# Performance work log

Hardware: AMD Instinct MI355X
Metric: run time of the kernel (lower is better)

## Reference

```python
import jax, jax.numpy as jnp
import numpy as np

B, T, U, E, P, C = 32, 4096, 1024, 512, 512, 4
LN_EPS = 1e-5


def setup_inputs() -> dict:
    key = jax.random.key(0)
    k = jax.random.split(key, 6)
    enc_out = jax.random.normal(k[0], (B, T, E), dtype=jnp.float32)
    pred_out = jax.random.normal(k[1], (B, U, P), dtype=jnp.float32)
    frame_label = jax.random.randint(k[2], (B, T), 0, C)
    frame_tlabel = jax.random.randint(k[3], (B, U), 0, C)
    # every emotion id appears in each sample's label list (dense [B, C])
    label = jnp.tile(jnp.arange(C), (B, 1))
    # LayerNorm params (torch defaults: weight=1, bias=0)
    norm_w = jnp.ones((E + P,), dtype=jnp.float32)
    norm_b = jnp.zeros((E + P,), dtype=jnp.float32)
    # Linear head params
    head_w = jax.random.normal(k[4], (C, E + P), dtype=jnp.float32) * 0.02
    head_b = jnp.zeros((C,), dtype=jnp.float32)
    return {
        "enc_out": enc_out, "pred_out": pred_out,
        "frame_label": frame_label, "frame_tlabel": frame_tlabel,
        "label": label,
        "norm_w": norm_w, "norm_b": norm_b,
        "head_w": head_w, "head_b": head_b,
    }


def _masked_mean(x, ids, n_cls):
    # x: [B, S, D]; ids: [B, S] -> per-class mean [B, C, D] via one-hot segment-sum
    onehot = (ids[:, :, None] == jnp.arange(n_cls)[None, None, :]).astype(x.dtype)  # [B,S,C]
    cnt = onehot.sum(axis=1)                                   # [B, C]
    summed = jnp.einsum('bsc,bsd->bcd', onehot, x)             # [B, C, D]
    return summed / jnp.maximum(cnt, 1.0)[..., None]


def reference(enc_out, pred_out, frame_label, frame_tlabel, label, norm_w, norm_b, head_w, head_b):
    n_cls = head_w.shape[0]
    enc_mean = _masked_mean(enc_out, frame_label, n_cls)    # [B, C, E]
    pred_mean = _masked_mean(pred_out, frame_tlabel, n_cls)  # [B, C, P]
    feat = jnp.concatenate([enc_mean, pred_mean], axis=-1)   # [B, C, E+P]
    # LayerNorm over last dim
    mu = feat.mean(axis=-1, keepdims=True)
    var = jnp.mean((feat - mu) ** 2, axis=-1, keepdims=True)
    feat_n = (feat - mu) / jnp.sqrt(var + LN_EPS) * norm_w + norm_b
    logits = jnp.einsum('bcd,nd->bcn', feat_n, head_w) + head_b  # [B, C, n_cls]
    logp = jax.nn.log_softmax(logits, axis=-1)
    # loss += -log_softmax(head(norm(cat)))[emo] for each emo in label[i]
    bb, ll = label.shape
    sel = logp[jnp.arange(bb)[:, None], label, label]  # [B, L]
    loss = -sel.sum() / (bb * ll)
    return loss
```

## Files before the change

### kernel.cpp

```cpp
#include <hip/hip_runtime.h>
#include <math.h>

#define C_CLS 4
#define D_HALF 512
#define D4 128
#define DFEAT 1024

__global__ void count_kernel(const int* __restrict__ fl, const int* __restrict__ ftl,
                             int T, int U, float* __restrict__ cnt) {
    int b = blockIdx.x;
    int which = blockIdx.y;
    const int* lab = (which == 0) ? (fl + (size_t)b * T) : (ftl + (size_t)b * U);
    int n = (which == 0) ? T : U;
    __shared__ int h[C_CLS];
    if (threadIdx.x < C_CLS) h[threadIdx.x] = 0;
    __syncthreads();
    for (int i = threadIdx.x; i < n; i += blockDim.x)
        atomicAdd(&h[lab[i]], 1);
    __syncthreads();
    if (threadIdx.x < C_CLS)
        cnt[((size_t)which * gridDim.x + b) * C_CLS + threadIdx.x] = (float)h[threadIdx.x];
}

__global__ void masked_sum_kernel(const float* __restrict__ x, const int* __restrict__ labels,
                                  float* __restrict__ partial, int Tlen, int splits) {
    int s = blockIdx.x;
    int b = blockIdx.y;
    int len = Tlen / splits;
    int t0 = s * len;
    int tx = threadIdx.x & 127;
    int ty = threadIdx.x >> 7;

    __shared__ int lab[1024];
    const int* labg = labels + (size_t)b * Tlen + t0;
    for (int i = threadIdx.x; i < len; i += 256) lab[i] = labg[i];
    __syncthreads();

    const float4* x4 = (const float4*)x + ((size_t)b * Tlen + t0) * D4 + tx;
    float4 acc[C_CLS];
#pragma unroll
    for (int k = 0; k < C_CLS; k++) acc[k] = make_float4(0.f, 0.f, 0.f, 0.f);

    for (int t = ty; t < len; t += 2) {
        float4 v = x4[(size_t)t * D4];
        int c = lab[t];
#pragma unroll
        for (int k = 0; k < C_CLS; k++) {
            float m = (c == k) ? 1.0f : 0.0f;
            acc[k].x = fmaf(v.x, m, acc[k].x);
            acc[k].y = fmaf(v.y, m, acc[k].y);
            acc[k].z = fmaf(v.z, m, acc[k].z);
            acc[k].w = fmaf(v.w, m, acc[k].w);
        }
    }

    __shared__ float4 cbuf[C_CLS][D4];
    if (ty == 1) {
#pragma unroll
        for (int k = 0; k < C_CLS; k++) cbuf[k][tx] = acc[k];
    }
    __syncthreads();
    if (ty == 0) {
        float4* out = (float4*)partial + (size_t)(b * splits + s) * C_CLS * D4 + tx;
#pragma unroll
        for (int k = 0; k < C_CLS; k++) {
            float4 o = acc[k], p = cbuf[k][tx];
            o.x += p.x; o.y += p.y; o.z += p.z; o.w += p.w;
            out[(size_t)k * D4] = o;
        }
    }
}

__device__ __forceinline__ float blockReduceSum256(float v) {
    __shared__ float red[4];
#pragma unroll
    for (int off = 32; off > 0; off >>= 1) v += __shfl_down(v, off);
    int wid = threadIdx.x >> 6, lane = threadIdx.x & 63;
    __syncthreads();
    if (lane == 0) red[wid] = v;
    __syncthreads();
    return red[0] + red[1] + red[2] + red[3];
}

__global__ void finalize_kernel(const float* __restrict__ enc_part,
                                const float* __restrict__ pred_part,
                                const float* __restrict__ cnt,
                                const float* __restrict__ norm_w, const float* __restrict__ norm_b,
                                const float* __restrict__ head_w, const float* __restrict__ head_b,
                                float* __restrict__ diag, int B, int SE, int SP) {
    int b = blockIdx.x;
    int c = blockIdx.y;
    __shared__ float feat[DFEAT];
    float cnt_e = fmaxf(cnt[((size_t)0 * B + b) * C_CLS + c], 1.0f);
    float cnt_p = fmaxf(cnt[((size_t)1 * B + b) * C_CLS + c], 1.0f);

    for (int d = threadIdx.x; d < D_HALF; d += 256) {
        float s = 0.f;
        for (int sp = 0; sp < SE; sp++)
            s += enc_part[((size_t)(b * SE + sp) * C_CLS + c) * D_HALF + d];
        feat[d] = s / cnt_e;
    }
    for (int d = threadIdx.x; d < D_HALF; d += 256) {
        float s = 0.f;
        for (int sp = 0; sp < SP; sp++)
            s += pred_part[((size_t)(b * SP + sp) * C_CLS + c) * D_HALF + d];
        feat[D_HALF + d] = s / cnt_p;
    }
    __syncthreads();

    float lsum = 0.f;
    for (int d = threadIdx.x; d < DFEAT; d += 256) lsum += feat[d];
    float mu = blockReduceSum256(lsum) * (1.0f / DFEAT);

    float lvar = 0.f;
    for (int d = threadIdx.x; d < DFEAT; d += 256) {
        float t = feat[d] - mu;
        lvar = fmaf(t, t, lvar);
    }
    float var = blockReduceSum256(lvar) * (1.0f / DFEAT);
    float rstd = rsqrtf(var + 1e-5f);

    float part[C_CLS] = {0.f, 0.f, 0.f, 0.f};
    for (int d = threadIdx.x; d < DFEAT; d += 256) {
        float fn = (feat[d] - mu) * rstd * norm_w[d] + norm_b[d];
#pragma unroll
        for (int n = 0; n < C_CLS; n++)
            part[n] = fmaf(fn, head_w[(size_t)n * DFEAT + d], part[n]);
    }
    float logits[C_CLS];
#pragma unroll
    for (int n = 0; n < C_CLS; n++)
        logits[n] = blockReduceSum256(part[n]) + head_b[n];

    if (threadIdx.x == 0) {
        float m = fmaxf(fmaxf(logits[0], logits[1]), fmaxf(logits[2], logits[3]));
        float se = 0.f;
#pragma unroll
        for (int n = 0; n < C_CLS; n++) se += expf(logits[n] - m);
        float lse = m + logf(se);
        diag[b * C_CLS + c] = logits[c] - lse;
    }
}

__global__ void loss_kernel(const float* __restrict__ diag, const int* __restrict__ label,
                            float* __restrict__ out, int B) {
    int i = threadIdx.x;
    float v = 0.f;
    if (i < B * C_CLS) {
        int b = i / C_CLS;
        int j = label[i];
        v = diag[b * C_CLS + j];
    }
#pragma unroll
    for (int off = 32; off > 0; off >>= 1) v += __shfl_down(v, off);
    __shared__ float red[2];
    int wid = i >> 6, lane = i & 63;
    if (lane == 0) red[wid] = v;
    __syncthreads();
    if (i == 0) out[0] = -(red[0] + red[1]) / (float)(B * C_CLS);
}

extern "C" void kernel_launch(void* const* d_in, const int* in_sizes, int n_in,
                              void* d_out, int out_size, void* d_ws, size_t ws_size,
                              hipStream_t stream) {
    const float* enc_out      = (const float*)d_in[0];
    const float* pred_out     = (const float*)d_in[1];
    const int*   frame_label  = (const int*)d_in[2];
    const int*   frame_tlabel = (const int*)d_in[3];
    const int*   label        = (const int*)d_in[4];
    const float* norm_w       = (const float*)d_in[5];
    const float* norm_b       = (const float*)d_in[6];
    const float* head_w       = (const float*)d_in[7];
    const float* head_b       = (const float*)d_in[8];
    float* out = (float*)d_out;

    const int B = 32, T = 4096, U = 1024;
    int SE = 16, SP = 8;
    auto need = [&](int se, int sp) -> size_t {
        return ((size_t)B * se * C_CLS * D_HALF + (size_t)B * sp * C_CLS * D_HALF
                + 2 * B * C_CLS + B * C_CLS) * sizeof(float);
    };
    while (need(SE, SP) > ws_size && SE > 4) { SE >>= 1; if (SP > 1) SP >>= 1; }

    float* ws        = (float*)d_ws;
    float* enc_part  = ws;
    float* pred_part = enc_part + (size_t)B * SE * C_CLS * D_HALF;
    float* cnt       = pred_part + (size_t)B * SP * C_CLS * D_HALF;
    float* diag      = cnt + 2 * B * C_CLS;

    count_kernel<<<dim3(B, 2), 256, 0, stream>>>(frame_label, frame_tlabel, T, U, cnt);
    masked_sum_kernel<<<dim3(SE, B), 256, 0, stream>>>(enc_out, frame_label, enc_part, T, SE);
    masked_sum_kernel<<<dim3(SP, B), 256, 0, stream>>>(pred_out, frame_tlabel, pred_part, U, SP);
    finalize_kernel<<<dim3(B, C_CLS), 256, 0, stream>>>(enc_part, pred_part, cnt,
                                                        norm_w, norm_b, head_w, head_b,
                                                        diag, B, SE, SP);
    loss_kernel<<<1, 128, 0, stream>>>(diag, label, out, B);
}
```

Baseline: 467.2 us.

## Fuse masked-sum launches, raise time splits, use register histograms for counts

The two masked-sum launches become one kernel that picks the enc or pred slice from a flat block index. The per-sample time splits go from 16/8 to 64/32, so far more blocks share the memory-bound streaming of the large inputs. The label count kernel now builds per-thread register histograms and does a few shared atomics per thread instead of one atomic per element. The cost is more partial sums, which the finalize kernel must reduce serially. The shared label buffer shrinks to match the shorter segments.

```diff
diff --git a/kernel.cpp b/kernel.cpp
--- a/kernel.cpp
+++ b/kernel.cpp
@@ -5,6 +5,7 @@
 #define D_HALF 512
 #define D4 128
 #define DFEAT 1024
+#define BB 32
 
 __global__ void count_kernel(const int* __restrict__ fl, const int* __restrict__ ftl,
                              int T, int U, float* __restrict__ cnt) {
@@ -15,23 +16,41 @@
     __shared__ int h[C_CLS];
     if (threadIdx.x < C_CLS) h[threadIdx.x] = 0;
     __syncthreads();
-    for (int i = threadIdx.x; i < n; i += blockDim.x)
-        atomicAdd(&h[lab[i]], 1);
+    int h0 = 0, h1 = 0, h2 = 0, h3 = 0;
+    for (int i = threadIdx.x; i < n; i += blockDim.x) {
+        int c = lab[i];
+        h0 += (c == 0); h1 += (c == 1); h2 += (c == 2); h3 += (c == 3);
+    }
+    if (h0) atomicAdd(&h[0], h0);
+    if (h1) atomicAdd(&h[1], h1);
+    if (h2) atomicAdd(&h[2], h2);
+    if (h3) atomicAdd(&h[3], h3);
     __syncthreads();
     if (threadIdx.x < C_CLS)
         cnt[((size_t)which * gridDim.x + b) * C_CLS + threadIdx.x] = (float)h[threadIdx.x];
 }
 
-__global__ void masked_sum_kernel(const float* __restrict__ x, const int* __restrict__ labels,
-                                  float* __restrict__ partial, int Tlen, int splits) {
-    int s = blockIdx.x;
-    int b = blockIdx.y;
+__global__ void masked_sum_fused(const float* __restrict__ enc, const float* __restrict__ pred,
+                                 const int* __restrict__ fl, const int* __restrict__ ftl,
+                                 float* __restrict__ enc_part, float* __restrict__ pred_part,
+                                 int T, int U, int SE, int SP) {
+    int bid = blockIdx.x;
+    const float* x; const int* labels; float* partial;
+    int Tlen, splits, b, s;
+    if (bid < BB * SE) {
+        x = enc; labels = fl; partial = enc_part; Tlen = T; splits = SE;
+        b = bid / SE; s = bid % SE;
+    } else {
+        int idx = bid - BB * SE;
+        x = pred; labels = ftl; partial = pred_part; Tlen = U; splits = SP;
+        b = idx / SP; s = idx % SP;
+    }
     int len = Tlen / splits;
     int t0 = s * len;
     int tx = threadIdx.x & 127;
     int ty = threadIdx.x >> 7;
 
-    __shared__ int lab[1024];
+    __shared__ int lab[256];
     const int* labg = labels + (size_t)b * Tlen + t0;
     for (int i = threadIdx.x; i < len; i += 256) lab[i] = labg[i];
     __syncthreads();
@@ -174,13 +193,13 @@
     const float* head_b       = (const float*)d_in[8];
     float* out = (float*)d_out;
 
-    const int B = 32, T = 4096, U = 1024;
-    int SE = 16, SP = 8;
+    const int B = BB, T = 4096, U = 1024;
+    int SE = 64, SP = 32;
     auto need = [&](int se, int sp) -> size_t {
         return ((size_t)B * se * C_CLS * D_HALF + (size_t)B * sp * C_CLS * D_HALF
                 + 2 * B * C_CLS + B * C_CLS) * sizeof(float);
     };
-    while (need(SE, SP) > ws_size && SE > 4) { SE >>= 1; if (SP > 1) SP >>= 1; }
+    while (need(SE, SP) > ws_size && SE > 16) { SE >>= 1; if (SP > 4) SP >>= 1; }
 
     float* ws        = (float*)d_ws;
     float* enc_part  = ws;
@@ -189,8 +208,9 @@
     float* diag      = cnt + 2 * B * C_CLS;
 
     count_kernel<<<dim3(B, 2), 256, 0, stream>>>(frame_label, frame_tlabel, T, U, cnt);
-    masked_sum_kernel<<<dim3(SE, B), 256, 0, stream>>>(enc_out, frame_label, enc_part, T, SE);
-    masked_sum_kernel<<<dim3(SP, B), 256, 0, stream>>>(pred_out, frame_tlabel, pred_part, U, SP);
+    masked_sum_fused<<<B * SE + B * SP, 256, 0, stream>>>(enc_out, pred_out,
+                                                          frame_label, frame_tlabel,
+                                                          enc_part, pred_part, T, U, SE, SP);
     finalize_kernel<<<dim3(B, C_CLS), 256, 0, stream>>>(enc_part, pred_part, cnt,
                                                         norm_w, norm_b, head_w, head_b,
                                                         diag, B, SE, SP);
```

Result: slower. 479.1 us (+2.5%).
